# Performance work log

Hardware: AMD Instinct MI355X
Metric: run time of the kernel (lower is better)

## Reference

```python
import jax, jax.numpy as jnp
import numpy as np

COMMIT_W = 0.25
EMA_DECAY = 0.99
EPS = 1e-5


def setup_inputs() -> dict:
    key = jax.random.key(0)
    k1, k2 = jax.random.split(key)
    B, T, D, K = 16, 1024, 512, 8192
    features = jax.random.normal(k1, (B, T, D), dtype=jnp.float32)
    # __init__ does uniform_(-1/K, 1/K) then ema_weight.copy_(embeddings)
    embeddings = jax.random.uniform(k2, (K, D), dtype=jnp.float32, minval=-1.0 / K, maxval=1.0 / K)
    ema_weight = embeddings
    ema_cluster_size = jnp.ones((K,), dtype=jnp.float32)
    return {"features": features, "embeddings": embeddings,
            "ema_cluster_size": ema_cluster_size, "ema_weight": ema_weight}


def reference(features, embeddings, ema_cluster_size, ema_weight):
    B, T, D = features.shape
    K = embeddings.shape[0]
    flat = features.reshape(-1, D)                      # [N, D]
    # Squared-distance expansion; argmin is identical to argmin of cdist.
    d2 = (jnp.sum(flat * flat, axis=1, keepdims=True)
          - 2.0 * flat @ embeddings.T
          + jnp.sum(embeddings * embeddings, axis=1))   # [N, K]
    indices = jnp.argmin(d2, axis=1)                    # [N]
    quantized = embeddings[indices].reshape(B, T, D)
    # Straight-through estimator
    quantized_st = features + jax.lax.stop_gradient(quantized - features)
    commitment = jnp.mean((features - jax.lax.stop_gradient(quantized_st)) ** 2)
    extra_losses = COMMIT_W * commitment
    # EMA codebook update (training mode); scatter-add instead of one-hot matmul
    ones = jnp.ones(indices.shape, dtype=flat.dtype)
    cluster_size = jax.ops.segment_sum(ones, indices, num_segments=K)          # [K]
    embed_sum = jax.ops.segment_sum(jax.lax.stop_gradient(flat), indices,
                                    num_segments=K)                            # [K, D]
    new_cs = EMA_DECAY * ema_cluster_size + (1.0 - EMA_DECAY) * cluster_size
    new_w = EMA_DECAY * ema_weight + (1.0 - EMA_DECAY) * embed_sum
    cs_norm = (new_cs + EPS) / (jnp.sum(new_cs) + K * EPS)
    new_embeddings = new_w / cs_norm[:, None]
    targets = indices.reshape(B, T)
    return quantized_st, targets, extra_losses, new_embeddings, new_cs, new_w
```

## Files before the change

kernel.cpp:

```cpp
#include <hip/hip_runtime.h>

typedef unsigned short u16;
typedef unsigned int   u32;
typedef unsigned long long u64;

constexpr int NROW  = 16384;
constexpr int DIM   = 512;
constexpr int KCODE = 8192;

constexpr int BM   = 128;
constexpr int BN   = 128;
constexpr int BK   = 32;
constexpr int LSTR = 36;

constexpr size_t Q_OFF = 0;
constexpr size_t T_OFF = 8388608;
constexpr size_t L_OFF = 8404992;
constexpr size_t E_OFF = 8404993;
constexpr size_t C_OFF = 12599297;
constexpr size_t W_OFF = 12607489;

constexpr size_t WS_KEYS   = 0;
constexpr size_t WS_CSIZE  = 131072;
constexpr size_t WS_COMMIT = 163840;
constexpr size_t WS_CSSUM  = 163844;
constexpr size_t WS_XNORM  = 196608;
constexpr size_t WS_ENORM  = 262144;
constexpr size_t WS_ESUM   = 327680;
constexpr size_t WS_NEEDED = WS_ESUM + (size_t)KCODE * DIM * 4;
constexpr size_t WS_FH = WS_NEEDED;
constexpr size_t WS_FL = WS_FH + (size_t)NROW * DIM * 2;
constexpr size_t WS_EH = WS_FL + (size_t)NROW * DIM * 2;
constexpr size_t WS_EL = WS_EH + (size_t)KCODE * DIM * 2;
constexpr size_t WS_BIG = WS_EL + (size_t)KCODE * DIM * 2;

__global__ void rownorm_kernel(const float* __restrict__ src, float* __restrict__ dst) {
    #pragma clang fp contract(off)
    __shared__ float s[4][DIM];
    __shared__ float rr[4][32];
    const int wave = threadIdx.x >> 6, lane = threadIdx.x & 63;
    const int row = blockIdx.x * 4 + wave;
    const float4* p = (const float4*)(src + (size_t)row * DIM);
    float4 v0 = p[lane];
    float4 v1 = p[lane + 64];
    *(float4*)&s[wave][lane * 4] = v0;
    *(float4*)&s[wave][(lane + 64) * 4] = v1;
    __syncthreads();
    if (lane < 32) {
        const int b = lane >> 3, j = lane & 7;
        const float* q = &s[wave][b * 128 + j];
        float x = q[0];
        float r = x * x;
        for (int t = 1; t < 16; ++t) {
            float y = q[8 * t];
            float py = y * y;
            r = r + py;
        }
        rr[wave][lane] = r;
    }
    __syncthreads();
    if (lane == 0) {
        const float* R = rr[wave];
        float B0 = ((R[0] + R[1]) + (R[2] + R[3])) + ((R[4] + R[5]) + (R[6] + R[7]));
        float B1 = ((R[8] + R[9]) + (R[10] + R[11])) + ((R[12] + R[13]) + (R[14] + R[15]));
        float B2 = ((R[16] + R[17]) + (R[18] + R[19])) + ((R[20] + R[21]) + (R[22] + R[23]));
        float B3 = ((R[24] + R[25]) + (R[26] + R[27])) + ((R[28] + R[29]) + (R[30] + R[31]));
        dst[row] = (B0 + B1) + (B2 + B3);
    }
}

typedef short bf16x8 __attribute__((ext_vector_type(8)));
typedef float f32x16 __attribute__((ext_vector_type(16)));

__device__ __forceinline__ bf16x8 frag_of(int4 t) {
    return __builtin_bit_cast(bf16x8, t);
}

__device__ __forceinline__ u32 bf16rne(float x) {
    u32 u = __float_as_uint(x);
    return (u + 0x7fffu + ((u >> 16) & 1u)) >> 16;
}

__device__ __forceinline__ void split4(float4 v, u32& hp0, u32& hp1, u32& lp0, u32& lp1) {
    u32 h0 = bf16rne(v.x), h1 = bf16rne(v.y), h2 = bf16rne(v.z), h3 = bf16rne(v.w);
    hp0 = h0 | (h1 << 16);
    hp1 = h2 | (h3 << 16);
    float r0 = v.x - __uint_as_float(h0 << 16);
    float r1 = v.y - __uint_as_float(h1 << 16);
    float r2 = v.z - __uint_as_float(h2 << 16);
    float r3 = v.w - __uint_as_float(h3 << 16);
    lp0 = bf16rne(r0) | (bf16rne(r1) << 16);
    lp1 = bf16rne(r2) | (bf16rne(r3) << 16);
}

__device__ __forceinline__ u64 packkey(float v, int code) {
    u32 vb = __float_as_uint(v);
    vb = (vb & 0x80000000u) ? ~vb : (vb | 0x80000000u);
    return ((u64)vb << 32) | (u32)code;
}

typedef __attribute__((address_space(1))) const void* gas_ptr;
typedef __attribute__((address_space(3))) void*       las_ptr;
__device__ __forceinline__ void gload16(const void* g, void* l) {
    __builtin_amdgcn_global_load_lds((gas_ptr)(unsigned long long)g,
                                     (las_ptr)(unsigned)(unsigned long long)l,
                                     16, 0, 0);
}

__global__ void split_kernel(const float* __restrict__ src,
                             u16* __restrict__ hi, u16* __restrict__ lo) {
    const size_t i = (size_t)blockIdx.x * 256 + threadIdx.x;
    const float4* p = (const float4*)src;
    float4 a = p[i * 2], b = p[i * 2 + 1];
    u32 ah0, ah1, al0, al1, bh0, bh1, bl0, bl1;
    split4(a, ah0, ah1, al0, al1);
    split4(b, bh0, bh1, bl0, bl1);
    ((uint4*)hi)[i] = make_uint4(ah0, ah1, bh0, bh1);
    ((uint4*)lo)[i] = make_uint4(al0, al1, bl0, bl1);
}

__attribute__((amdgpu_waves_per_eu(3, 3)))
__launch_bounds__(256)
__global__ void argmin_ps_kernel(const u16* __restrict__ fH, const u16* __restrict__ fL,
                                 const u16* __restrict__ eH, const u16* __restrict__ eL,
                                 const float* __restrict__ xnorm,
                                 const float* __restrict__ enorm,
                                 u64* __restrict__ keys) {
    __shared__ int4 sAh[512], sAl[512], sBh[512], sBl[512];
    __shared__ float sXn[BM], sEn[BN];

    const int tid = threadIdx.x;
    const int swz = ((int)blockIdx.x & 7) * 1024 + ((int)blockIdx.x >> 3);
    const int cp = swz & 63;
    const int rp = swz >> 6;
    const int row0 = rp * BM;
    const int code0 = cp * BN;

    if (tid < BM) sXn[tid] = xnorm[row0 + tid];
    else          sEn[tid - BM] = enorm[code0 + (tid - BM)];

    const int lane = tid & 63;
    const int wv = tid >> 6;
    const int wr = wv & 1, wc = wv >> 1;
    const int c5 = lane & 31, hgrp = lane >> 5;

    const int4* fH4 = (const int4*)fH;
    const int4* fL4 = (const int4*)fL;
    const int4* eH4 = (const int4*)eH;
    const int4* eL4 = (const int4*)eL;

    size_t goA[2], goB[2];
    int gb[2];
    #pragma unroll
    for (int h = 0; h < 2; ++h) {
        const int g = h * 4 + wv;
        const int i = g * 64 + lane;
        const int r = i >> 8, rb = (i >> 7) & 1, k8 = (i >> 5) & 3, c5i = i & 31;
        const int rl = r * 64 + rb * 32 + c5i;
        goA[h] = (size_t)(row0 + rl) * 64 + k8;
        goB[h] = (size_t)(code0 + rl) * 64 + k8;
        gb[h] = g * 64;
    }

    f32x16 acc[2][2] = {};

    #pragma unroll 1
    for (int kt = 0; kt < DIM / BK; ++kt) {
        __syncthreads();
        #pragma unroll
        for (int h = 0; h < 2; ++h) {
            gload16(fH4 + goA[h] + kt * 4, (void*)&sAh[gb[h]]);
            gload16(fL4 + goA[h] + kt * 4, (void*)&sAl[gb[h]]);
            gload16(eH4 + goB[h] + kt * 4, (void*)&sBh[gb[h]]);
            gload16(eL4 + goB[h] + kt * 4, (void*)&sBl[gb[h]]);
        }
        asm volatile("s_waitcnt vmcnt(0)" ::: "memory");
        __syncthreads();
        #pragma unroll
        for (int s = 0; s < 2; ++s) {
            const int k8 = s * 2 + hgrp;
            bf16x8 ah[2], al[2], bh[2], bl[2];
            #pragma unroll
            for (int i = 0; i < 2; ++i) {
                ah[i] = frag_of(sAh[((2 * wr + i) * 4 + k8) * 32 + c5]);
                al[i] = frag_of(sAl[((2 * wr + i) * 4 + k8) * 32 + c5]);
                bh[i] = frag_of(sBh[((2 * wc + i) * 4 + k8) * 32 + c5]);
                bl[i] = frag_of(sBl[((2 * wc + i) * 4 + k8) * 32 + c5]);
            }
            #pragma unroll
            for (int i = 0; i < 2; ++i) {
                #pragma unroll
                for (int j = 0; j < 2; ++j) {
                    acc[i][j] = __builtin_amdgcn_mfma_f32_32x32x16_bf16(ah[i], bh[j], acc[i][j], 0, 0, 0);
                    acc[i][j] = __builtin_amdgcn_mfma_f32_32x32x16_bf16(ah[i], bl[j], acc[i][j], 0, 0, 0);
                    acc[i][j] = __builtin_amdgcn_mfma_f32_32x32x16_bf16(al[i], bh[j], acc[i][j], 0, 0, 0);
                }
            }
        }
    }

    #pragma unroll
    for (int i = 0; i < 2; ++i) {
        #pragma unroll
        for (int r = 0; r < 16; ++r) {
            const int rowt = 64 * wr + 32 * i + (r & 3) + 8 * (r >> 2) + 4 * hgrp;
            const float xv = sXn[rowt];
            const int ct0 = 64 * wc + c5;
            float v0 = fmaf(-2.0f, acc[i][0][r], xv) + sEn[ct0];
            float v1 = fmaf(-2.0f, acc[i][1][r], xv) + sEn[ct0 + 32];
            u64 ka = packkey(v0, code0 + ct0);
            u64 kb = packkey(v1, code0 + ct0 + 32);
            u64 key = (kb < ka) ? kb : ka;
            #pragma unroll
            for (int m = 1; m < 32; m <<= 1) {
                u64 o = __shfl_xor(key, m, 64);
                if (o < key) key = o;
            }
            if (c5 == 0) atomicMin(&keys[row0 + rowt], key);
        }
    }
}

__launch_bounds__(256, 3)
__global__ void argmin_conv_kernel(const float* __restrict__ feat,
                                   const float* __restrict__ emb,
                                   const float* __restrict__ xnorm,
                                   const float* __restrict__ enorm,
                                   u64* __restrict__ keys) {
    __shared__ u16 sAh[BM][LSTR], sAl[BM][LSTR], sBh[BN][LSTR], sBl[BN][LSTR];
    __shared__ float sXn[BM], sEn[BN];

    const int tid = threadIdx.x;
    const int swz = ((int)blockIdx.x & 7) * 1024 + ((int)blockIdx.x >> 3);
    const int cp = swz & 63;
    const int rp = swz >> 6;
    const int row0 = rp * BM;
    const int code0 = cp * BN;

    if (tid < BM) sXn[tid] = xnorm[row0 + tid];
    else          sEn[tid - BM] = enorm[code0 + (tid - BM)];

    const int srow = tid >> 3;
    const int scol = (tid & 7) * 4;
    const float* aBase = feat + (size_t)row0 * DIM;
    const float* bBase = emb + (size_t)code0 * DIM;

    float4 pa[4], pb[4];
    #pragma unroll
    for (int l = 0; l < 4; ++l) {
        pa[l] = *(const float4*)&aBase[(size_t)(srow + 32 * l) * DIM + scol];
        pb[l] = *(const float4*)&bBase[(size_t)(srow + 32 * l) * DIM + scol];
    }

    const int lane = tid & 63;
    const int wv = tid >> 6;
    const int wr = wv & 1, wc = wv >> 1;
    const int c5 = lane & 31, hgrp = lane >> 5;

    f32x16 acc[2][2] = {};

    #pragma unroll 1
    for (int kt = 0; kt < DIM / BK; ++kt) {
        __syncthreads();
        #pragma unroll
        for (int l = 0; l < 4; ++l) {
            u32 h0, h1, q0, q1;
            split4(pa[l], h0, h1, q0, q1);
            *(uint2*)&sAh[srow + 32 * l][scol] = make_uint2(h0, h1);
            *(uint2*)&sAl[srow + 32 * l][scol] = make_uint2(q0, q1);
            split4(pb[l], h0, h1, q0, q1);
            *(uint2*)&sBh[srow + 32 * l][scol] = make_uint2(h0, h1);
            *(uint2*)&sBl[srow + 32 * l][scol] = make_uint2(q0, q1);
        }
        __syncthreads();
        if (kt + 1 < DIM / BK) {
            const int k0 = (kt + 1) * BK;
            #pragma unroll
            for (int l = 0; l < 4; ++l) {
                pa[l] = *(const float4*)&aBase[(size_t)(srow + 32 * l) * DIM + k0 + scol];
                pb[l] = *(const float4*)&bBase[(size_t)(srow + 32 * l) * DIM + k0 + scol];
            }
        }
        #pragma unroll
        for (int s = 0; s < 2; ++s) {
            const int kk = s * 16 + hgrp * 8;
            bf16x8 ah[2], al[2], bh[2], bl[2];
            #pragma unroll
            for (int i = 0; i < 2; ++i) {
                uint2 a0 = *(const uint2*)&sAh[64 * wr + 32 * i + c5][kk];
                uint2 a1 = *(const uint2*)&sAh[64 * wr + 32 * i + c5][kk + 4];
                ah[i] = frag_of(make_int4(a0.x, a0.y, a1.x, a1.y));
                uint2 c0 = *(const uint2*)&sAl[64 * wr + 32 * i + c5][kk];
                uint2 c1 = *(const uint2*)&sAl[64 * wr + 32 * i + c5][kk + 4];
                al[i] = frag_of(make_int4(c0.x, c0.y, c1.x, c1.y));
                uint2 b0 = *(const uint2*)&sBh[64 * wc + 32 * i + c5][kk];
                uint2 b1 = *(const uint2*)&sBh[64 * wc + 32 * i + c5][kk + 4];
                bh[i] = frag_of(make_int4(b0.x, b0.y, b1.x, b1.y));
                uint2 d0 = *(const uint2*)&sBl[64 * wc + 32 * i + c5][kk];
                uint2 d1 = *(const uint2*)&sBl[64 * wc + 32 * i + c5][kk + 4];
                bl[i] = frag_of(make_int4(d0.x, d0.y, d1.x, d1.y));
            }
            #pragma unroll
            for (int i = 0; i < 2; ++i) {
                #pragma unroll
                for (int j = 0; j < 2; ++j) {
                    acc[i][j] = __builtin_amdgcn_mfma_f32_32x32x16_bf16(ah[i], bh[j], acc[i][j], 0, 0, 0);
                    acc[i][j] = __builtin_amdgcn_mfma_f32_32x32x16_bf16(ah[i], bl[j], acc[i][j], 0, 0, 0);
                    acc[i][j] = __builtin_amdgcn_mfma_f32_32x32x16_bf16(al[i], bh[j], acc[i][j], 0, 0, 0);
                }
            }
        }
    }

    #pragma unroll
    for (int i = 0; i < 2; ++i) {
        #pragma unroll
        for (int r = 0; r < 16; ++r) {
            const int rowt = 64 * wr + 32 * i + (r & 3) + 8 * (r >> 2) + 4 * hgrp;
            const float xv = sXn[rowt];
            const int ct0 = 64 * wc + c5;
            float v0 = fmaf(-2.0f, acc[i][0][r], xv) + sEn[ct0];
            float v1 = fmaf(-2.0f, acc[i][1][r], xv) + sEn[ct0 + 32];
            u64 ka = packkey(v0, code0 + ct0);
            u64 kb = packkey(v1, code0 + ct0 + 32);
            u64 key = (kb < ka) ? kb : ka;
            #pragma unroll
            for (int m = 1; m < 32; m <<= 1) {
                u64 o = __shfl_xor(key, m, 64);
                if (o < key) key = o;
            }
            if (c5 == 0) atomicMin(&keys[row0 + rowt], key);
        }
    }
}

__global__ void gather_kernel(const float* __restrict__ feat,
                              const float* __restrict__ emb,
                              const unsigned long long* __restrict__ keys,
                              float* __restrict__ qout,
                              float* __restrict__ targets,
                              float* __restrict__ esum,
                              float* __restrict__ csize,
                              float* __restrict__ commit) {
    const int row = blockIdx.x;
    const int code = (int)(keys[row] & 0x7fffffffu);
    const int d = threadIdx.x * 2;
    float2 f = *(const float2*)&feat[(size_t)row * DIM + d];
    float2 q = *(const float2*)&emb[(size_t)code * DIM + d];
    float2 qst;
    qst.x = f.x + (q.x - f.x);
    qst.y = f.y + (q.y - f.y);
    *(float2*)&qout[(size_t)row * DIM + d] = qst;
    float dx = f.x - qst.x, dy = f.y - qst.y;
    float local = dx * dx + dy * dy;
    #pragma unroll
    for (int off = 32; off; off >>= 1) local += __shfl_down(local, off, 64);
    __shared__ float wsum[4];
    int lane = threadIdx.x & 63, wv = threadIdx.x >> 6;
    if (lane == 0) wsum[wv] = local;
    __syncthreads();
    if (threadIdx.x == 0) {
        atomicAdd(commit, wsum[0] + wsum[1] + wsum[2] + wsum[3]);
        atomicAdd(&csize[code], 1.0f);
        targets[row] = (float)code;
    }
    atomicAdd(&esum[(size_t)code * DIM + d], f.x);
    atomicAdd(&esum[(size_t)code * DIM + d + 1], f.y);
}

__global__ void newcs_kernel(const float* __restrict__ ema_cs,
                             const float* __restrict__ csize,
                             float* __restrict__ out_cs,
                             float* __restrict__ cs_sum,
                             const float* __restrict__ commit,
                             float* __restrict__ out_loss) {
    int i = blockIdx.x * 256 + threadIdx.x;
    float v = 0.99f * ema_cs[i] + 0.01f * csize[i];
    out_cs[i] = v;
    float s = v;
    #pragma unroll
    for (int off = 32; off; off >>= 1) s += __shfl_down(s, off, 64);
    __shared__ float wsum[4];
    int lane = threadIdx.x & 63, wv = threadIdx.x >> 6;
    if (lane == 0) wsum[wv] = s;
    __syncthreads();
    if (threadIdx.x == 0)
        atomicAdd(cs_sum, wsum[0] + wsum[1] + wsum[2] + wsum[3]);
    if (blockIdx.x == 0 && threadIdx.x == 0)
        out_loss[0] = 0.25f * commit[0] / 8388608.0f;
}

__global__ void final_kernel(const float* __restrict__ ema_w,
                             const float* __restrict__ esum,
                             const float* __restrict__ new_cs,
                             const float* __restrict__ cs_sum,
                             float* __restrict__ out_w,
                             float* __restrict__ out_emb) {
    size_t i4 = ((size_t)blockIdx.x * 256 + threadIdx.x) * 4;
    int k = (int)(i4 >> 9);
    float S = cs_sum[0] + (float)KCODE * 1e-5f;
    float4 es = *(const float4*)&esum[i4];
    float4 ew = *(const float4*)&ema_w[i4];
    float w0 = 0.99f * ew.x + 0.01f * es.x;
    float w1 = 0.99f * ew.y + 0.01f * es.y;
    float w2 = 0.99f * ew.z + 0.01f * es.z;
    float w3 = 0.99f * ew.w + 0.01f * es.w;
    out_w[i4 + 0] = w0; out_w[i4 + 1] = w1; out_w[i4 + 2] = w2; out_w[i4 + 3] = w3;
    float scale = S / (new_cs[k] + 1e-5f);
    out_emb[i4 + 0] = w0 * scale; out_emb[i4 + 1] = w1 * scale;
    out_emb[i4 + 2] = w2 * scale; out_emb[i4 + 3] = w3 * scale;
}

extern "C" void kernel_launch(void* const* d_in, const int* in_sizes, int n_in,
                              void* d_out, int out_size, void* d_ws, size_t ws_size,
                              hipStream_t stream) {
    const float* feat   = (const float*)d_in[0];
    const float* emb    = (const float*)d_in[1];
    const float* ema_cs = (const float*)d_in[2];
    const float* ema_w  = (const float*)d_in[3];
    float* out = (float*)d_out;
    char* ws = (char*)d_ws;
    if (ws_size < WS_NEEDED) return;

    u64* keys     = (u64*)(ws + WS_KEYS);
    float* csize  = (float*)(ws + WS_CSIZE);
    float* commit = (float*)(ws + WS_COMMIT);
    float* cssum  = (float*)(ws + WS_CSSUM);
    float* xnorm  = (float*)(ws + WS_XNORM);
    float* enorm  = (float*)(ws + WS_ENORM);
    float* esum   = (float*)(ws + WS_ESUM);

    (void)hipMemsetAsync(ws + WS_KEYS, 0xFF, (size_t)NROW * 8, stream);
    (void)hipMemsetAsync(ws + WS_CSIZE, 0, WS_CSSUM + 4 - WS_CSIZE, stream);
    (void)hipMemsetAsync(ws + WS_ESUM, 0, (size_t)KCODE * DIM * 4, stream);

    rownorm_kernel<<<NROW / 4, 256, 0, stream>>>(feat, xnorm);
    rownorm_kernel<<<KCODE / 4, 256, 0, stream>>>(emb, enorm);

    if (ws_size >= WS_BIG) {
        u16* fH = (u16*)(ws + WS_FH);
        u16* fL = (u16*)(ws + WS_FL);
        u16* eH = (u16*)(ws + WS_EH);
        u16* eL = (u16*)(ws + WS_EL);
        split_kernel<<<(NROW * DIM) / (256 * 8), 256, 0, stream>>>(feat, fH, fL);
        split_kernel<<<(KCODE * DIM) / (256 * 8), 256, 0, stream>>>(emb, eH, eL);
        argmin_ps_kernel<<<(NROW / BM) * (KCODE / BN), 256, 0, stream>>>(fH, fL, eH, eL,
                                                                         xnorm, enorm, keys);
    } else {
        argmin_conv_kernel<<<(NROW / BM) * (KCODE / BN), 256, 0, stream>>>(feat, emb,
                                                                           xnorm, enorm, keys);
    }

    gather_kernel<<<NROW, 256, 0, stream>>>(feat, emb, keys, out + Q_OFF, out + T_OFF,
                                            esum, csize, commit);
    newcs_kernel<<<KCODE / 256, 256, 0, stream>>>(ema_cs, csize, out + C_OFF, cssum, commit, out + L_OFF);
    final_kernel<<<KCODE * DIM / 1024, 256, 0, stream>>>(ema_w, esum, out + C_OFF, cssum,
                                                         out + W_OFF, out + E_OFF);
}
```

Baseline: 1.052 ms.

## Double-buffer LDS tiles in argmin GEMM to overlap loads with MFMA

After: 1.127 ms. 7.2% more time.

```diff
diff --git a/kernel.cpp b/kernel.cpp
--- a/kernel.cpp
+++ b/kernel.cpp
@@ -119,14 +119,14 @@
     ((uint4*)lo)[i] = make_uint4(al0, al1, bl0, bl1);
 }
 
-__attribute__((amdgpu_waves_per_eu(3, 3)))
+__attribute__((amdgpu_waves_per_eu(2, 2)))
 __launch_bounds__(256)
 __global__ void argmin_ps_kernel(const u16* __restrict__ fH, const u16* __restrict__ fL,
                                  const u16* __restrict__ eH, const u16* __restrict__ eL,
                                  const float* __restrict__ xnorm,
                                  const float* __restrict__ enorm,
                                  u64* __restrict__ keys) {
-    __shared__ int4 sAh[512], sAl[512], sBh[512], sBl[512];
+    __shared__ int4 sAh[2][512], sAl[2][512], sBh[2][512], sBl[2][512];
     __shared__ float sXn[BM], sEn[BN];
 
     const int tid = threadIdx.x;
@@ -164,28 +164,26 @@
 
     f32x16 acc[2][2] = {};
 
-    #pragma unroll 1
-    for (int kt = 0; kt < DIM / BK; ++kt) {
-        __syncthreads();
+    auto STAGE = [&](int buf, int kt) {
         #pragma unroll
         for (int h = 0; h < 2; ++h) {
-            gload16(fH4 + goA[h] + kt * 4, (void*)&sAh[gb[h]]);
-            gload16(fL4 + goA[h] + kt * 4, (void*)&sAl[gb[h]]);
-            gload16(eH4 + goB[h] + kt * 4, (void*)&sBh[gb[h]]);
-            gload16(eL4 + goB[h] + kt * 4, (void*)&sBl[gb[h]]);
-        }
-        asm volatile("s_waitcnt vmcnt(0)" ::: "memory");
-        __syncthreads();
+            gload16(fH4 + goA[h] + kt * 4, (void*)&sAh[buf][gb[h]]);
+            gload16(fL4 + goA[h] + kt * 4, (void*)&sAl[buf][gb[h]]);
+            gload16(eH4 + goB[h] + kt * 4, (void*)&sBh[buf][gb[h]]);
+            gload16(eL4 + goB[h] + kt * 4, (void*)&sBl[buf][gb[h]]);
+        }
+    };
+    auto COMPUTE = [&](int buf) {
         #pragma unroll
         for (int s = 0; s < 2; ++s) {
             const int k8 = s * 2 + hgrp;
             bf16x8 ah[2], al[2], bh[2], bl[2];
             #pragma unroll
             for (int i = 0; i < 2; ++i) {
-                ah[i] = frag_of(sAh[((2 * wr + i) * 4 + k8) * 32 + c5]);
-                al[i] = frag_of(sAl[((2 * wr + i) * 4 + k8) * 32 + c5]);
-                bh[i] = frag_of(sBh[((2 * wc + i) * 4 + k8) * 32 + c5]);
-                bl[i] = frag_of(sBl[((2 * wc + i) * 4 + k8) * 32 + c5]);
+                ah[i] = frag_of(sAh[buf][((2 * wr + i) * 4 + k8) * 32 + c5]);
+                al[i] = frag_of(sAl[buf][((2 * wr + i) * 4 + k8) * 32 + c5]);
+                bh[i] = frag_of(sBh[buf][((2 * wc + i) * 4 + k8) * 32 + c5]);
+                bl[i] = frag_of(sBl[buf][((2 * wc + i) * 4 + k8) * 32 + c5]);
             }
             #pragma unroll
             for (int i = 0; i < 2; ++i) {
@@ -197,7 +195,22 @@
                 }
             }
         }
-    }
+    };
+
+    STAGE(0, 0);
+    asm volatile("s_waitcnt vmcnt(0)" ::: "memory");
+    __syncthreads();
+
+    int cur = 0;
+    #pragma unroll 1
+    for (int kt = 0; kt < DIM / BK - 1; ++kt) {
+        STAGE(cur ^ 1, kt + 1);
+        COMPUTE(cur);
+        asm volatile("s_waitcnt vmcnt(0)" ::: "memory");
+        __syncthreads();
+        cur ^= 1;
+    }
+    COMPUTE(cur);
 
     #pragma unroll
     for (int i = 0; i < 2; ++i) {
```
